# Performance work log

Measured on AMD Instinct MI355X. Metric: run time of the kernel, lower is better.

## Reference

```python
import jax, jax.numpy as jnp
import numpy as np

B, IN, OUT, G, K = 8192, 2048, 2048, 5, 3
EPS = 1e-8


def b_spline_basis(x, grid, k=K):
    # x: [B, in], grid: [in, G]
    Gn = grid.shape[1]
    diff = x[:, :, None] - grid[None, :, :]                      # [B, in, G]
    basis = ((diff >= 0) & (diff < 1)).astype(x.dtype)           # order-0 indicator
    for order in range(1, k + 1):
        js = np.arange(Gn - order)
        i2 = np.minimum(js + order, Gn - 1)       # clamp of original OOB index
        i3 = np.minimum(js + order + 1, Gn - 1)   # clamp of original OOB index
        prev = basis
        # note: original uses (diff[:,:,j] - grid[:,j]) = x - 2*grid[:,j]; kept faithfully
        t1 = (diff[:, :, js] - grid[:, js]) / (grid[:, i2] - grid[:, js] + EPS) * prev[:, :, js]
        t2 = (grid[:, i3] - diff[:, :, js]) / (grid[:, i3] - grid[:, js + 1] + EPS) * prev[:, :, js + 1]
        basis = basis.at[:, :, js].set(t1 + t2)
    return basis


def setup_inputs() -> dict:
    key = jax.random.key(0)
    k1, k2, k3, k4, k5 = jax.random.split(key, 5)
    bound = 1.0 / np.sqrt(IN)
    x = jax.random.normal(k1, (B, IN), dtype=jnp.float32)
    base_weight = jax.random.uniform(k2, (OUT, IN), dtype=jnp.float32, minval=-bound, maxval=bound)
    base_bias = jax.random.uniform(k3, (OUT,), dtype=jnp.float32, minval=-bound, maxval=bound)
    spline_weight = jax.random.uniform(k4, (OUT, IN, G), dtype=jnp.float32, minval=-0.1, maxval=0.1)
    grid = jax.random.uniform(k5, (IN, G), dtype=jnp.float32, minval=-1.0, maxval=1.0)
    return {"x": x, "base_weight": base_weight, "base_bias": base_bias,
            "spline_weight": spline_weight, "grid": grid}


def reference(x, base_weight, base_bias, spline_weight, grid):
    base_output = x @ base_weight.T + base_bias                   # [B, out]
    spline_basis = b_spline_basis(x, grid, K)                     # [B, in, G]
    spline_output = jnp.einsum('big,oig->bo', spline_basis, spline_weight)
    return base_output + spline_output
```

## Files before the change

kernel.cpp:

```cpp
#include <hip/hip_runtime.h>
#include <hip/hip_bf16.h>

#define EPS 1e-8f

constexpr int B_   = 8192;
constexpr int IN_  = 2048;
constexpr int OUT_ = 2048;
constexpr int KA_  = IN_ * 6;
constexpr int NT_  = KA_ / 64;

typedef __bf16 bf16x8 __attribute__((ext_vector_type(8)));
typedef float  f32x4  __attribute__((ext_vector_type(4)));

__device__ __forceinline__ ushort f2bf(float f) {
    union { float f; uint u; } v; v.f = f;
    uint u = v.u;
    uint r = u + 0x7fffu + ((u >> 16) & 1u);
    return (ushort)(r >> 16);
}

__device__ __forceinline__ void gload16(const void* g, void* l) {
    __builtin_amdgcn_global_load_lds(
        (const __attribute__((address_space(1))) void*)g,
        (__attribute__((address_space(3))) void*)l,
        16, 0, 0);
}

__global__ __launch_bounds__(256) void stage_a(const float* __restrict__ x,
                                               const float* __restrict__ grid,
                                               ushort* __restrict__ A) {
    __shared__ __attribute__((aligned(16))) ushort pack[1536];
    const int tid = threadIdx.x;
    const int b0  = blockIdx.x * 16;
    const int i0  = blockIdx.y * 256;
    const int i   = i0 + tid;

    float g[5];
#pragma unroll
    for (int j = 0; j < 5; ++j) g[j] = grid[i * 5 + j];

    float r1[9], r2[9];
    {
        int t = 0;
#pragma unroll
        for (int o = 1; o <= 3; ++o) {
#pragma unroll
            for (int j = 0; j < 5 - o; ++j) {
                int i2 = min(j + o, 4);
                int i3 = min(j + o + 1, 4);
                r1[t] = 1.0f / (g[i2] - g[j] + EPS);
                r2[t] = 1.0f / (g[i3] - g[j + 1] + EPS);
                ++t;
            }
        }
    }

    for (int r = 0; r < 16; ++r) {
        const int b = b0 + r;
        float xv = x[(size_t)b * IN_ + i];
        float diff[5], bas[5];
#pragma unroll
        for (int j = 0; j < 5; ++j) {
            diff[j] = xv - g[j];
            bas[j]  = (diff[j] >= 0.0f && diff[j] < 1.0f) ? 1.0f : 0.0f;
        }
        int t = 0;
#pragma unroll
        for (int o = 1; o <= 3; ++o) {
            float nb[4];
#pragma unroll
            for (int j = 0; j < 5 - o; ++j) {
                int i3 = min(j + o + 1, 4);
                float t1 = (diff[j] - g[j]) * r1[t] * bas[j];
                float t2 = (g[i3] - diff[j]) * r2[t] * bas[j + 1];
                nb[j] = t1 + t2;
                ++t;
            }
#pragma unroll
            for (int j = 0; j < 5 - o; ++j) bas[j] = nb[j];
        }

        pack[tid * 6 + 0] = f2bf(xv);
#pragma unroll
        for (int j = 0; j < 5; ++j) pack[tid * 6 + 1 + j] = f2bf(bas[j]);
        __syncthreads();
        {
            const uint* ps = (const uint*)pack;
            uint* pd = (uint*)(A + (size_t)b * KA_ + (size_t)i0 * 6);
#pragma unroll
            for (int j = 0; j < 3; ++j) pd[tid + j * 256] = ps[tid + j * 256];
        }
        __syncthreads();
    }
}

__global__ __launch_bounds__(256) void stage_w(const float* __restrict__ bw,
                                               const float* __restrict__ sw,
                                               ushort* __restrict__ W) {
    __shared__ __attribute__((aligned(16))) float  ssh[1280];
    __shared__ __attribute__((aligned(16))) ushort wsh[1536];
    const int tid = threadIdx.x;
    const int o   = blockIdx.x;
    const int i0  = blockIdx.y * 256;

    const float* sp = sw + ((size_t)o * IN_ + i0) * 5;
    for (int j = tid; j < 1280; j += 256) ssh[j] = sp[j];
    float bwv = bw[(size_t)o * IN_ + i0 + tid];
    __syncthreads();

    wsh[tid * 6] = f2bf(bwv);
#pragma unroll
    for (int j = 0; j < 5; ++j) wsh[tid * 6 + 1 + j] = f2bf(ssh[tid * 5 + j]);
    __syncthreads();

    const uint* ps = (const uint*)wsh;
    uint* pd = (uint*)(W + (size_t)o * KA_ + (size_t)i0 * 6);
#pragma unroll
    for (int j = 0; j < 3; ++j) pd[tid + j * 256] = ps[tid + j * 256];
}

__global__ __launch_bounds__(512, 2) void gemm_kan8(const ushort* __restrict__ A,
                                                    const ushort* __restrict__ W,
                                                    const float* __restrict__ bias,
                                                    float* __restrict__ out) {
    __shared__ __attribute__((aligned(16))) char lds[2][2][32768];

    const int tid  = threadIdx.x;
    const int lane = tid & 63;
    const int wave = tid >> 6;
    const int wr   = wave >> 2;
    const int wc   = wave & 3;

    uint bid = blockIdx.x;
    uint swz = (bid & 7u) * 32u + (bid >> 3);
    const int bm = (int)(swz >> 3);
    const int bn = (int)(swz & 7u);

    const uint lhi16 = ((uint)lane >> 4) * 16u;
    const uint swx   = ((uint)lane & 7u) << 4;
    uint aro[8], wro[4];
#pragma unroll
    for (int m = 0; m < 8; ++m) aro[m] = (uint)(wr * 128 + m * 16 + (lane & 15)) * 128u;
#pragma unroll
    for (int n = 0; n < 4; ++n) wro[n] = (uint)(wc * 64 + n * 16 + (lane & 15)) * 128u;

    const uint srow0 = (uint)wave * 8u + ((uint)lane >> 3);
    const uint srow1 = srow0 + 64u;
    const uint gcol  = (((uint)lane & 7u) ^ (((uint)lane >> 3) & 7u)) * 8u;
    const ushort* pA0 = A + (size_t)bm * 256 * KA_ + (size_t)srow0 * KA_ + gcol;
    const ushort* pA1 = A + (size_t)bm * 256 * KA_ + (size_t)srow1 * KA_ + gcol;
    const ushort* pW0 = W + (size_t)bn * 256 * KA_ + (size_t)srow0 * KA_ + gcol;
    const ushort* pW1 = W + (size_t)bn * 256 * KA_ + (size_t)srow1 * KA_ + gcol;
    const uint c0off = (uint)wave * 1024u;
    const uint c1off = c0off + 8192u;

    f32x4 acc[8][4];
#pragma unroll
    for (int m = 0; m < 8; ++m)
#pragma unroll
        for (int n = 0; n < 4; ++n)
            acc[m][n] = (f32x4){0.f, 0.f, 0.f, 0.f};

#define DSR(base, ro, kh) (*(const bf16x8*)((base) + (ro) + (((kh) * 64u + lhi16) ^ swx)))

#define STAGE(s, mat, h, kk, PT0, PT1) do {                                   \
        uint kc_ = (uint)((kk) < NT_ ? (kk) : 0);                             \
        size_t go_ = (size_t)(h) * 128 * KA_ + (size_t)kc_ * 64;              \
        gload16(PT0 + go_, &lds[s][mat][(h) * 16384 + c0off]);                \
        gload16(PT1 + go_, &lds[s][mat][(h) * 16384 + c1off]);                \
    } while (0)

#define RDA(dst, base, mb) do {                                               \
        _Pragma("unroll") for (int m_ = 0; m_ < 4; ++m_) {                    \
            dst[m_][0] = DSR(base, aro[(mb) + m_], 0);                        \
            dst[m_][1] = DSR(base, aro[(mb) + m_], 1); } } while (0)

#define RDB4(dst, base) do {                                                  \
        _Pragma("unroll") for (int n_ = 0; n_ < 4; ++n_) {                    \
            dst[n_][0] = DSR(base, wro[n_], 0);                               \
            dst[n_][1] = DSR(base, wro[n_], 1); } } while (0)

#define MIDBAR() do { __builtin_amdgcn_s_barrier();                           \
        asm volatile("s_waitcnt lgkmcnt(0)" ::: "memory");                    \
        __builtin_amdgcn_sched_barrier(0); } while (0)

#define MFMA32(AF, BF, MB) do {                                               \
        __builtin_amdgcn_s_setprio(1);                                        \
        _Pragma("unroll") for (int m_ = 0; m_ < 4; ++m_)                      \
        _Pragma("unroll") for (int n_ = 0; n_ < 4; ++n_)                      \
            acc[(MB)+m_][n_] = __builtin_amdgcn_mfma_f32_16x16x32_bf16(       \
                AF[m_][0], BF[n_][0], acc[(MB)+m_][n_], 0, 0, 0);             \
        _Pragma("unroll") for (int m_ = 0; m_ < 4; ++m_)                      \
        _Pragma("unroll") for (int n_ = 0; n_ < 4; ++n_)                      \
            acc[(MB)+m_][n_] = __builtin_amdgcn_mfma_f32_16x16x32_bf16(       \
                AF[m_][1], BF[n_][1], acc[(MB)+m_][n_], 0, 0, 0);             \
        __builtin_amdgcn_s_setprio(0); } while (0)

#define ENDBAR() __builtin_amdgcn_s_barrier()

    const char* As0 = lds[0][0]; const char* Ws0 = lds[0][1];
    const char* As1 = lds[1][0]; const char* Ws1 = lds[1][1];

    STAGE(0, 0, 0, 0, pA0, pA1);
    STAGE(0, 0, 1, 0, pA0, pA1);
    STAGE(0, 1, 0, 0, pW0, pW1);
    STAGE(0, 1, 1, 0, pW0, pW1);
    STAGE(1, 1, 0, 1, pW0, pW1);
    STAGE(1, 1, 1, 1, pW0, pW1);
    asm volatile("s_waitcnt vmcnt(4)" ::: "memory");
    __builtin_amdgcn_s_barrier();

    bf16x8 a0[4][2], a1[4][2], b[4][2];

    for (int it = 0; it < NT_ / 2; ++it) {
        const int t1 = 2 * it + 1;
        RDA(a0, As0, 0); RDB4(b, Ws0);
        STAGE(1, 0, 0, t1, pA0, pA1);
        STAGE(1, 0, 1, t1, pA0, pA1);
        MIDBAR(); MFMA32(a0, b, 0); ENDBAR();
        RDA(a1, As0, 4);
        STAGE(0, 1, 0, t1 + 1, pW0, pW1);
        STAGE(0, 1, 1, t1 + 1, pW0, pW1);
        asm volatile("s_waitcnt vmcnt(4)" ::: "memory");
        MIDBAR(); MFMA32(a1, b, 4); ENDBAR();
        RDA(a0, As1, 0); RDB4(b, Ws1);
        STAGE(0, 0, 0, t1 + 1, pA0, pA1);
        STAGE(0, 0, 1, t1 + 1, pA0, pA1);
        MIDBAR(); MFMA32(a0, b, 0); ENDBAR();
        RDA(a1, As1, 4);
        STAGE(1, 1, 0, t1 + 2, pW0, pW1);
        STAGE(1, 1, 1, t1 + 2, pW0, pW1);
        asm volatile("s_waitcnt vmcnt(4)" ::: "memory");
        MIDBAR(); MFMA32(a1, b, 4); ENDBAR();
    }

    const int orow0 = bm * 256 + wr * 128;
    const int ocol0 = bn * 256 + wc * 64;
#pragma unroll
    for (int n = 0; n < 4; ++n) {
        int c = ocol0 + n * 16 + (lane & 15);
        float bv = bias[c];
#pragma unroll
        for (int m = 0; m < 8; ++m) {
            int r0 = orow0 + m * 16 + ((lane >> 4) << 2);
#pragma unroll
            for (int j = 0; j < 4; ++j)
                out[(size_t)(r0 + j) * OUT_ + c] = acc[m][n][j] + bv;
        }
    }
#undef DSR
#undef STAGE
#undef RDA
#undef RDB4
#undef MIDBAR
#undef MFMA32
#undef ENDBAR
}

__global__ __launch_bounds__(256) void kan_fallback(const float* __restrict__ x,
                                                    const float* __restrict__ bw,
                                                    const float* __restrict__ bb,
                                                    const float* __restrict__ sw,
                                                    const float* __restrict__ grid,
                                                    float* __restrict__ out) {
    __shared__ float ash[16 * 384];
    const int tid = threadIdx.x;
    const int o   = blockIdx.x * 256 + tid;
    const int b0  = blockIdx.y * 16;
    float acc[16];
#pragma unroll
    for (int r = 0; r < 16; ++r) acc[r] = 0.0f;

    for (int ic = 0; ic < IN_; ic += 64) {
        __syncthreads();
        for (int p = tid; p < 1024; p += 256) {
            int r = p >> 6, ii = p & 63;
            int i = ic + ii;
            float xv = x[(size_t)(b0 + r) * IN_ + i];
            float g[5];
#pragma unroll
            for (int j = 0; j < 5; ++j) g[j] = grid[i * 5 + j];
            float diff[5], bas[5];
#pragma unroll
            for (int j = 0; j < 5; ++j) {
                diff[j] = xv - g[j];
                bas[j]  = (diff[j] >= 0.0f && diff[j] < 1.0f) ? 1.0f : 0.0f;
            }
#pragma unroll
            for (int oo = 1; oo <= 3; ++oo) {
                float nb[4];
#pragma unroll
                for (int j = 0; j < 5 - oo; ++j) {
                    int i2 = min(j + oo, 4);
                    int i3 = min(j + oo + 1, 4);
                    nb[j] = (diff[j] - g[j]) / (g[i2] - g[j] + EPS) * bas[j]
                          + (g[i3] - diff[j]) / (g[i3] - g[j + 1] + EPS) * bas[j + 1];
                }
#pragma unroll
                for (int j = 0; j < 5 - oo; ++j) bas[j] = nb[j];
            }
            float* ap = &ash[r * 384 + ii * 6];
            ap[0] = xv;
#pragma unroll
            for (int j = 0; j < 5; ++j) ap[1 + j] = bas[j];
        }
        __syncthreads();
        for (int ii = 0; ii < 64; ++ii) {
            int i = ic + ii;
            float w0 = bw[(size_t)o * IN_ + i];
            const float* swp = sw + ((size_t)o * IN_ + i) * 5;
            float w1 = swp[0], w2 = swp[1], w3 = swp[2], w4 = swp[3], w5 = swp[4];
#pragma unroll
            for (int r = 0; r < 16; ++r) {
                const float* a = &ash[r * 384 + ii * 6];
                acc[r] += a[0] * w0 + a[1] * w1 + a[2] * w2
                        + a[3] * w3 + a[4] * w4 + a[5] * w5;
            }
        }
    }
    float bv = bb[o];
#pragma unroll
    for (int r = 0; r < 16; ++r)
        out[(size_t)(b0 + r) * OUT_ + o] = acc[r] + bv;
}

extern "C" void kernel_launch(void* const* d_in, const int* in_sizes, int n_in,
                              void* d_out, int out_size, void* d_ws, size_t ws_size,
                              hipStream_t stream) {
    (void)in_sizes; (void)n_in; (void)out_size;
    const float* x    = (const float*)d_in[0];
    const float* bw   = (const float*)d_in[1];
    const float* bb   = (const float*)d_in[2];
    const float* sw   = (const float*)d_in[3];
    const float* grid = (const float*)d_in[4];
    float* out = (float*)d_out;

    const size_t needA = (size_t)B_ * KA_ * sizeof(ushort);
    const size_t needW = (size_t)OUT_ * KA_ * sizeof(ushort);

    if (ws_size >= needA + needW) {
        ushort* A = (ushort*)d_ws;
        ushort* W = A + (size_t)B_ * KA_;
        stage_a<<<dim3(B_ / 16, IN_ / 256), 256, 0, stream>>>(x, grid, A);
        stage_w<<<dim3(OUT_, IN_ / 256), 256, 0, stream>>>(bw, sw, W);
        gemm_kan8<<<dim3(256), 512, 0, stream>>>(A, W, bb, out);
    } else {
        kan_fallback<<<dim3(OUT_ / 256, B_ / 16), 256, 0, stream>>>(x, bw, bb, sw, grid, out);
    }
}
```

Before: 429.2 us.

## Load W fragments directly from global into registers, bypassing LDS

The GEMM no longer stages the W tile through LDS. Each wave loads its own B fragments straight from global memory into registers, double-buffered across k-steps, and only A stays in LDS. This halves LDS footprint and removes the LDS write/read traffic for W, but W loads are now uncoalesced per-lane and redundant across the two wave rows. The loop is also split into finer 16-MFMA phases with more barriers and vmcnt(0) waits, which may expose global latency.

```diff
diff --git a/kernel.cpp b/kernel.cpp
--- a/kernel.cpp
+++ b/kernel.cpp
@@ -119,11 +119,11 @@
     for (int j = 0; j < 3; ++j) pd[tid + j * 256] = ps[tid + j * 256];
 }
 
-__global__ __launch_bounds__(512, 2) void gemm_kan8(const ushort* __restrict__ A,
+__global__ __launch_bounds__(512, 2) void gemm_kanw(const ushort* __restrict__ A,
                                                     const ushort* __restrict__ W,
                                                     const float* __restrict__ bias,
                                                     float* __restrict__ out) {
-    __shared__ __attribute__((aligned(16))) char lds[2][2][32768];
+    __shared__ __attribute__((aligned(16))) char lds[2][32768];
 
     const int tid  = threadIdx.x;
     const int lane = tid & 63;
@@ -138,22 +138,23 @@
 
     const uint lhi16 = ((uint)lane >> 4) * 16u;
     const uint swx   = ((uint)lane & 7u) << 4;
-    uint aro[8], wro[4];
+    uint aro[8];
 #pragma unroll
     for (int m = 0; m < 8; ++m) aro[m] = (uint)(wr * 128 + m * 16 + (lane & 15)) * 128u;
-#pragma unroll
-    for (int n = 0; n < 4; ++n) wro[n] = (uint)(wc * 64 + n * 16 + (lane & 15)) * 128u;
 
     const uint srow0 = (uint)wave * 8u + ((uint)lane >> 3);
-    const uint srow1 = srow0 + 64u;
     const uint gcol  = (((uint)lane & 7u) ^ (((uint)lane >> 3) & 7u)) * 8u;
     const ushort* pA0 = A + (size_t)bm * 256 * KA_ + (size_t)srow0 * KA_ + gcol;
-    const ushort* pA1 = A + (size_t)bm * 256 * KA_ + (size_t)srow1 * KA_ + gcol;
-    const ushort* pW0 = W + (size_t)bn * 256 * KA_ + (size_t)srow0 * KA_ + gcol;
-    const ushort* pW1 = W + (size_t)bn * 256 * KA_ + (size_t)srow1 * KA_ + gcol;
+    const ushort* pA1 = pA0 + (size_t)64 * KA_;
     const uint c0off = (uint)wave * 1024u;
     const uint c1off = c0off + 8192u;
 
+    const ushort* pw[4];
+#pragma unroll
+    for (int n = 0; n < 4; ++n)
+        pw[n] = W + (size_t)(bn * 256 + wc * 64 + n * 16 + (lane & 15)) * KA_
+                  + ((lane >> 4) * 8);
+
     f32x4 acc[8][4];
 #pragma unroll
     for (int m = 0; m < 8; ++m)
@@ -163,75 +164,67 @@
 
 #define DSR(base, ro, kh) (*(const bf16x8*)((base) + (ro) + (((kh) * 64u + lhi16) ^ swx)))
 
-#define STAGE(s, mat, h, kk, PT0, PT1) do {                                   \
+#define STAGE(s, h, kk) do {                                                  \
         uint kc_ = (uint)((kk) < NT_ ? (kk) : 0);                             \
         size_t go_ = (size_t)(h) * 128 * KA_ + (size_t)kc_ * 64;              \
-        gload16(PT0 + go_, &lds[s][mat][(h) * 16384 + c0off]);                \
-        gload16(PT1 + go_, &lds[s][mat][(h) * 16384 + c1off]);                \
+        gload16(pA0 + go_, &lds[s][(h) * 16384 + c0off]);                     \
+        gload16(pA1 + go_, &lds[s][(h) * 16384 + c1off]);                     \
     } while (0)
 
-#define RDA(dst, base, mb) do {                                               \
-        _Pragma("unroll") for (int m_ = 0; m_ < 4; ++m_) {                    \
-            dst[m_][0] = DSR(base, aro[(mb) + m_], 0);                        \
-            dst[m_][1] = DSR(base, aro[(mb) + m_], 1); } } while (0)
-
-#define RDB4(dst, base) do {                                                  \
-        _Pragma("unroll") for (int n_ = 0; n_ < 4; ++n_) {                    \
-            dst[n_][0] = DSR(base, wro[n_], 0);                               \
-            dst[n_][1] = DSR(base, wro[n_], 1); } } while (0)
+#define WL(dst, OFF) do {                                                     \
+        _Pragma("unroll") for (int n_ = 0; n_ < 4; ++n_)                      \
+        _Pragma("unroll") for (int k_ = 0; k_ < 2; ++k_)                      \
+            dst[n_][k_] = *(const bf16x8*)(pw[n_] + (OFF) + k_ * 32);         \
+    } while (0)
+
+#define RD4(base, MB, KH) do {                                                \
+        _Pragma("unroll") for (int m_ = 0; m_ < 4; ++m_)                      \
+            a[m_] = DSR(base, aro[(MB) + m_], KH); } while (0)
 
 #define MIDBAR() do { __builtin_amdgcn_s_barrier();                           \
         asm volatile("s_waitcnt lgkmcnt(0)" ::: "memory");                    \
         __builtin_amdgcn_sched_barrier(0); } while (0)
 
-#define MFMA32(AF, BF, MB) do {                                               \
+#define MFMA16(MB, BF, KH) do {                                               \
         __builtin_amdgcn_s_setprio(1);                                        \
         _Pragma("unroll") for (int m_ = 0; m_ < 4; ++m_)                      \
         _Pragma("unroll") for (int n_ = 0; n_ < 4; ++n_)                      \
             acc[(MB)+m_][n_] = __builtin_amdgcn_mfma_f32_16x16x32_bf16(       \
-                AF[m_][0], BF[n_][0], acc[(MB)+m_][n_], 0, 0, 0);             \
-        _Pragma("unroll") for (int m_ = 0; m_ < 4; ++m_)                      \
-        _Pragma("unroll") for (int n_ = 0; n_ < 4; ++n_)                      \
-            acc[(MB)+m_][n_] = __builtin_amdgcn_mfma_f32_16x16x32_bf16(       \
-                AF[m_][1], BF[n_][1], acc[(MB)+m_][n_], 0, 0, 0);             \
+                a[m_], BF[n_][KH], acc[(MB)+m_][n_], 0, 0, 0);                \
         __builtin_amdgcn_s_setprio(0); } while (0)
 
+#define VMC0() asm volatile("s_waitcnt vmcnt(0)" ::: "memory")
 #define ENDBAR() __builtin_amdgcn_s_barrier()
 
-    const char* As0 = lds[0][0]; const char* Ws0 = lds[0][1];
-    const char* As1 = lds[1][0]; const char* Ws1 = lds[1][1];
-
-    STAGE(0, 0, 0, 0, pA0, pA1);
-    STAGE(0, 0, 1, 0, pA0, pA1);
-    STAGE(0, 1, 0, 0, pW0, pW1);
-    STAGE(0, 1, 1, 0, pW0, pW1);
-    STAGE(1, 1, 0, 1, pW0, pW1);
-    STAGE(1, 1, 1, 1, pW0, pW1);
-    asm volatile("s_waitcnt vmcnt(4)" ::: "memory");
+    const char* As0 = lds[0];
+    const char* As1 = lds[1];
+
+    bf16x8 a[4], bW0[4][2], bW1[4][2];
+
+    STAGE(0, 0, 0);
+    STAGE(0, 1, 0);
+    WL(bW0, 0);
+    VMC0();
     __builtin_amdgcn_s_barrier();
-
-    bf16x8 a0[4][2], a1[4][2], b[4][2];
 
     for (int it = 0; it < NT_ / 2; ++it) {
         const int t1 = 2 * it + 1;
-        RDA(a0, As0, 0); RDB4(b, Ws0);
-        STAGE(1, 0, 0, t1, pA0, pA1);
-        STAGE(1, 0, 1, t1, pA0, pA1);
-        MIDBAR(); MFMA32(a0, b, 0); ENDBAR();
-        RDA(a1, As0, 4);
-        STAGE(0, 1, 0, t1 + 1, pW0, pW1);
-        STAGE(0, 1, 1, t1 + 1, pW0, pW1);
-        asm volatile("s_waitcnt vmcnt(4)" ::: "memory");
-        MIDBAR(); MFMA32(a1, b, 4); ENDBAR();
-        RDA(a0, As1, 0); RDB4(b, Ws1);
-        STAGE(0, 0, 0, t1 + 1, pA0, pA1);
-        STAGE(0, 0, 1, t1 + 1, pA0, pA1);
-        MIDBAR(); MFMA32(a0, b, 0); ENDBAR();
-        RDA(a1, As1, 4);
-        STAGE(1, 1, 0, t1 + 2, pW0, pW1);
-        STAGE(1, 1, 1, t1 + 2, pW0, pW1);
-        asm volatile("s_waitcnt vmcnt(4)" ::: "memory");
-        MIDBAR(); MFMA32(a1, b, 4); ENDBAR();
+        const int off5 = (2 * it + 2 < NT_) ? 128 : 128 - KA_;
+        STAGE(1, 0, t1);
+        STAGE(1, 1, t1);
+        WL(bW1, 64);
+        RD4(As0, 0, 0); MIDBAR(); MFMA16(0, bW0, 0); ENDBAR();
+        RD4(As0, 0, 1); MIDBAR(); MFMA16(0, bW0, 1); ENDBAR();
+        RD4(As0, 4, 0); MIDBAR(); MFMA16(4, bW0, 0); ENDBAR();
+        RD4(As0, 4, 1); MIDBAR(); MFMA16(4, bW0, 1); VMC0(); ENDBAR();
+        STAGE(0, 0, t1 + 1);
+        STAGE(0, 1, t1 + 1);
+        WL(bW0, off5);
+        RD4(As1, 0, 0); MIDBAR(); MFMA16(0, bW1, 0); ENDBAR();
+        RD4(As1, 0, 1); MIDBAR(); MFMA16(0, bW1, 1); ENDBAR();
+        RD4(As1, 4, 0); MIDBAR(); MFMA16(4, bW1, 0); ENDBAR();
+        RD4(As1, 4, 1); MIDBAR(); MFMA16(4, bW1, 1); VMC0(); ENDBAR();
+        pw[0] += 128; pw[1] += 128; pw[2] += 128; pw[3] += 128;
     }
 
     const int orow0 = bm * 256 + wr * 128;
@@ -250,10 +243,11 @@
     }
 #undef DSR
 #undef STAGE
-#undef RDA
-#undef RDB4
+#undef WL
+#undef RD4
 #undef MIDBAR
-#undef MFMA32
+#undef MFMA16
+#undef VMC0
 #undef ENDBAR
 }
 
@@ -343,7 +337,7 @@
         ushort* W = A + (size_t)B_ * KA_;
         stage_a<<<dim3(B_ / 16, IN_ / 256), 256, 0, stream>>>(x, grid, A);
         stage_w<<<dim3(OUT_, IN_ / 256), 256, 0, stream>>>(bw, sw, W);
-        gemm_kan8<<<dim3(256), 512, 0, stream>>>(A, W, bb, out);
+        gemm_kanw<<<dim3(256), 512, 0, stream>>>(A, W, bb, out);
     } else {
         kan_fallback<<<dim3(OUT_ / 256, B_ / 16), 256, 0, stream>>>(x, bw, bb, sw, grid, out);
     }
```

Result: slower. 725.3 us (+69.0%).
